# Performance work log

Measured on AMD Instinct MI355X. Metric: run time of the kernel, lower is better.

Reference implementation:

```python
import jax, jax.numpy as jnp
import numpy as np

B = 128      # number of swarms
NA = 64      # agents per swarm (na)
D = 8        # input feature dim
RD = 128     # attention hidden dim r
H = 16       # output channels h (l = sqrt(h) = 4)


def setup_inputs() -> dict:
    key = jax.random.key(0)
    ks = jax.random.split(key, 16)
    x = jax.random.normal(ks[0], (B * NA, D, NA), dtype=jnp.float32)
    L = jax.random.randint(ks[1], (B * NA, D, NA), 0, 2).astype(jnp.float32)
    p = lambda k, shp: jax.random.normal(k, shp, dtype=jnp.float32)
    return {
        "x": x, "L": L,
        "Aq": p(ks[2], (RD, D)), "Ak": p(ks[3], (RD, D)), "Av": p(ks[4], (RD, D)),
        "Aq1": p(ks[5], (RD, RD)), "Ak1": p(ks[6], (RD, RD)), "Av1": p(ks[7], (RD, RD)),
        "Aq5": p(ks[8], (RD, RD)), "Ak5": p(ks[9], (RD, RD)), "Av5": p(ks[10], (RD, RD)),
        "Ao": p(ks[11], (RD, RD)), "Ao1": p(ks[12], (RD, RD)), "Ao5": p(ks[13], (H, RD)),
    }


def _attn(Xin, Aq, Ak, Av, sqrt_nn):
    # Xin: (b, f, n); Aq/Ak/Av: (r, f); sqrt_nn: (b, 1, 1)
    Q = jax.nn.sigmoid(jnp.einsum('rf,bfn->bnr', Aq, Xin))   # Q already transposed
    K = jax.nn.sigmoid(jnp.einsum('rf,bfn->brn', Ak, Xin))
    V = jax.nn.sigmoid(jnp.einsum('rf,bfn->bnr', Av, Xin))
    S = jnp.einsum('bnr,brm->bnm', Q, K) / sqrt_nn           # (b, n, n)
    A = jax.nn.softmax(S, axis=2)
    return jnp.einsum('bnm,bmr->brn', A, V)                  # o^T: (b, r, n)


def _kron_eye2(A):
    # torch.kron(A, eye(2)) per batch: (B, n, n) -> (B, 2n, 2n)
    Bq, n, _ = A.shape
    I2 = jnp.eye(2, dtype=A.dtype)
    return (A[:, :, None, :, None] * I2[None, :, None, :]).reshape(Bq, 2 * n, 2 * n)


def reference(x, L, Aq, Ak, Av, Aq1, Ak1, Av1, Aq5, Ak5, Av5, Ao, Ao1, Ao5):
    na = x.shape[2]
    Bsw = x.shape[0] // na
    num_nb = jnp.sum((L[:, 0, :] >= 1.0).astype(jnp.float32), axis=1) + 1.0
    sqrt_nn = jnp.sqrt(num_nb)[:, None, None]                # (Bx, 1, 1)

    o = _attn(x, Aq, Ak, Av, sqrt_nn)
    R = jax.nn.silu(jnp.einsum('sr,brn->bsn', Ao, o))
    o = _attn(R, Aq1, Ak1, Av1, sqrt_nn)
    R = jax.nn.silu(jnp.einsum('sr,brn->bsn', Ao1, o))
    o = _attn(R, Aq5, Ak5, Av5, sqrt_nn)
    R = jax.nn.silu(jnp.einsum('hr,brn->bhn', Ao5, o))       # (Bx, 16, na)

    blk = lambda a, b: R[:, a:b, :].sum(axis=1).reshape(Bsw, na, na)
    R11 = _kron_eye2(blk(0, 4))
    R12 = _kron_eye2(blk(4, 8))
    R21 = _kron_eye2(blk(8, 12))
    R22 = _kron_eye2(blk(12, 16))
    # block matrix [[R11, R12], [R21, R22]] -> (Bsw, 4na, 4na)
    Rfull = jnp.concatenate(
        (jnp.concatenate((R11, R21), axis=1), jnp.concatenate((R12, R22), axis=1)),
        axis=2)

    Rfull = Rfull ** 2
    Rupper = Rfull + jnp.swapaxes(Rfull, 1, 2)
    n_tot = 4 * na
    Dg = jnp.eye(n_tot, dtype=Rupper.dtype)
    Rdiag = Rupper * (1.0 - Dg)                              # diag zeroed
    Rout = Dg * Rupper                                       # keep diag only
    rowsum = jnp.sum(Rdiag, axis=2)[:, :, None]              # (Bsw, n, 1)
    return Rout + Dg * rowsum - Rdiag
```

## Files before the change

kernel.cpp:

```cpp
#include <hip/hip_runtime.h>

typedef _Float16 f16;
typedef __attribute__((ext_vector_type(8))) _Float16 h8v;
typedef __attribute__((ext_vector_type(4))) float f4v;
typedef __attribute__((ext_vector_type(16))) float f16acc;

#define OFF_WQ  0
#define OFF_WK  2048
#define OFF_WV  4096
#define OFF_AQ1 6144
#define OFF_AK1 22528
#define OFF_AV1 38912
#define OFF_AQ5 55296
#define OFF_AK5 71680
#define OFF_AV5 88064
#define OFF_AO  104448
#define OFF_AO1 120832
#define OFF_AO5 137216
#define WTS_TOTAL 139264

#define P2 136
#define P1 72

__device__ __forceinline__ f4v mfma16_(h8v a, h8v b, f4v c) {
  return __builtin_amdgcn_mfma_f32_16x16x32_f16(a, b, c, 0, 0, 0);
}
__device__ __forceinline__ f16acc mfma32_(h8v a, h8v b, f16acc c) {
  return __builtin_amdgcn_mfma_f32_32x32x16_f16(a, b, c, 0, 0, 0);
}
__device__ __forceinline__ float rcp_(float x) { return __builtin_amdgcn_rcpf(x); }
__device__ __forceinline__ float ex2_(float x) {
#if __has_builtin(__builtin_amdgcn_exp2f)
  return __builtin_amdgcn_exp2f(x);
#else
  return __expf(x * 0.6931471805599453f);
#endif
}
__device__ __forceinline__ unsigned int pk2(float a, float b) {
  __fp16 __attribute__((ext_vector_type(2))) h2 = __builtin_amdgcn_cvt_pkrtz(a, b);
  return *reinterpret_cast<unsigned int*>(&h2);
}
__device__ __forceinline__ f16acc zero16() {
  f16acc z;
  #pragma unroll
  for (int i = 0; i < 16; ++i) z[i] = 0.f;
  return z;
}

template<int ACT>
__device__ __forceinline__ unsigned long long pack4act(float a, float b, float c, float d) {
  float v[4] = {a, b, c, d};
  #pragma unroll
  for (int j = 0; j < 4; ++j) {
    float t = v[j];
    if (ACT == 0)      t = rcp_(1.0f + ex2_(t));
    else if (ACT == 1) t = t * rcp_(1.0f + ex2_(t * -1.44269504f));
    v[j] = t;
  }
  union { unsigned long long u64; unsigned int u32[2]; } u;
  u.u32[0] = pk2(v[0], v[1]);
  u.u32[1] = pk2(v[2], v[3]);
  return u.u64;
}

template<int NKK>
__device__ __forceinline__ void qkv_ph(const f16* __restrict__ Wq,
                                       const f16* __restrict__ Wk,
                                       const f16* __restrict__ Wv,
                                       const f16* __restrict__ Xt,
                                       f16* __restrict__ Qt, f16* __restrict__ Kt,
                                       f16* __restrict__ Vb, int w, int lane)
{
  const int l31 = lane & 31, lh = lane >> 5;
  const int rt = w >> 1, ct = w & 1;
  const int xbase = (ct * 32 + l31) * P2 + lh * 8;
  f16acc aq = zero16(), ak = zero16(), av = zero16();
  #pragma unroll
  for (int kk = 0; kk < NKK; ++kk) {
    h8v xf = *(const h8v*)(Xt + xbase + kk * 16);
    const int fo = (rt * NKK + kk) * 512 + lane * 8;
    h8v fq = *(const h8v*)(Wq + fo);
    h8v fk = *(const h8v*)(Wk + fo);
    h8v fv = *(const h8v*)(Wv + fo);
    aq = mfma32_(fq, xf, aq);
    ak = mfma32_(fk, xf, ak);
    av = mfma32_(xf, fv, av);
  }
  const int nrow = (ct * 32 + l31) * P2;
  const int vrow = (rt * 32 + l31) * P1 + ct * 32 + lh * 4;
  #pragma unroll
  for (int q = 0; q < 4; ++q) {
    const int rr = rt * 32 + q * 8 + lh * 4;
    *(unsigned long long*)(Qt + nrow + rr) =
        pack4act<0>(aq[4*q], aq[4*q+1], aq[4*q+2], aq[4*q+3]);
    *(unsigned long long*)(Kt + nrow + rr) =
        pack4act<0>(ak[4*q], ak[4*q+1], ak[4*q+2], ak[4*q+3]);
    *(unsigned long long*)(Vb + vrow + q * 8) =
        pack4act<0>(av[4*q], av[4*q+1], av[4*q+2], av[4*q+3]);
  }
}

__device__ __forceinline__ void softmax_ph(const f16* __restrict__ Qt,
                                           const f16* __restrict__ Kt,
                                           f16* Ps, float* __restrict__ ssum,
                                           float is2, int w, int lane)
{
  const int lrow = lane & 15, lk = lane >> 4;
  const int nst = w & 3, mh = w >> 2;
  const int n = nst * 16 + lrow;
  h8v bq[4];
  #pragma unroll
  for (int kk = 0; kk < 4; ++kk)
    bq[kk] = *(const h8v*)(Qt + n * P2 + kk * 32 + lk * 8);
  f4v acc[2];
  #pragma unroll
  for (int t = 0; t < 2; ++t) {
    const int mt = mh * 2 + t;
    acc[t] = (f4v){0.f, 0.f, 0.f, 0.f};
    #pragma unroll
    for (int kk = 0; kk < 4; ++kk) {
      h8v a = *(const h8v*)(Kt + (mt * 16 + lrow) * P2 + kk * 32 + lk * 8);
      acc[t] = mfma16_(a, bq[kk], acc[t]);
    }
  }
  float sm = 0.f;
  #pragma unroll
  for (int t = 0; t < 2; ++t)
    #pragma unroll
    for (int j = 0; j < 4; ++j) { acc[t][j] = ex2_(acc[t][j] * is2); sm += acc[t][j]; }
  sm += __shfl_xor(sm, 16);
  sm += __shfl_xor(sm, 32);
  if (lk == 0) ssum[mh * 64 + n] = sm;
  __syncthreads();
  const float inv = rcp_(ssum[n] + ssum[64 + n]);
  #pragma unroll
  for (int t = 0; t < 2; ++t) {
    const int mt = mh * 2 + t;
    union { unsigned long long u64; unsigned int u32[2]; } u;
    u.u32[0] = pk2(acc[t][0] * inv, acc[t][1] * inv);
    u.u32[1] = pk2(acc[t][2] * inv, acc[t][3] * inv);
    *(unsigned long long*)(Ps + n * P1 + mt * 16 + lk * 4) = u.u64;
  }
}

__device__ __forceinline__ void pv_ph(const f16* __restrict__ Vb,
                                      const f16* __restrict__ Ps,
                                      f16* __restrict__ Ot, int w, int lane)
{
  const int l31 = lane & 31, lh = lane >> 5;
  const int rt = w >> 1, ct = w & 1;
  f16acc acc = zero16();
  #pragma unroll
  for (int kk = 0; kk < 4; ++kk) {
    h8v a = *(const h8v*)(Vb + (rt * 32 + l31) * P1 + kk * 16 + lh * 8);
    h8v b = *(const h8v*)(Ps + (ct * 32 + l31) * P1 + kk * 16 + lh * 8);
    acc = mfma32_(a, b, acc);
  }
  const int nrow = (ct * 32 + l31) * P2;
  #pragma unroll
  for (int q = 0; q < 4; ++q)
    *(unsigned long long*)(Ot + nrow + rt * 32 + q * 8 + lh * 4) =
        pack4act<2>(acc[4*q], acc[4*q+1], acc[4*q+2], acc[4*q+3]);
}

__device__ __forceinline__ void ao_ph(const f16* __restrict__ Ao,
                                      const f16* __restrict__ Ot,
                                      f16* __restrict__ Rt, int w, int lane)
{
  const int l31 = lane & 31, lh = lane >> 5;
  const int st = w >> 1, ct = w & 1;
  f16acc acc = zero16();
  #pragma unroll
  for (int kk = 0; kk < 8; ++kk) {
    h8v a = *(const h8v*)(Ao + (st * 8 + kk) * 512 + lane * 8);
    h8v b = *(const h8v*)(Ot + (ct * 32 + l31) * P2 + kk * 16 + lh * 8);
    acc = mfma32_(a, b, acc);
  }
  const int nrow = (ct * 32 + l31) * P2;
  #pragma unroll
  for (int q = 0; q < 4; ++q)
    *(unsigned long long*)(Rt + nrow + st * 32 + q * 8 + lh * 4) =
        pack4act<1>(acc[4*q], acc[4*q+1], acc[4*q+2], acc[4*q+3]);
}

__device__ __forceinline__ void final_ph(const f16* __restrict__ Ao5g,
                                         const f16* __restrict__ Ot,
                                         float* __restrict__ Mw, int b, int w, int lane)
{
  const int lrow = lane & 15, lk = lane >> 4;
  h8v a[4];
  #pragma unroll
  for (int kk = 0; kk < 4; ++kk)
    a[kk] = *(const h8v*)(Ao5g + lrow * 128 + kk * 32 + lk * 8);
  const int n = 16 * w + lrow;
  f4v acc = {0.f, 0.f, 0.f, 0.f};
  #pragma unroll
  for (int kk = 0; kk < 4; ++kk) {
    h8v bb = *(const h8v*)(Ot + n * P2 + kk * 32 + lk * 8);
    acc = mfma16_(a[kk], bb, acc);
  }
  float msum = 0.f;
  #pragma unroll
  for (int j = 0; j < 4; ++j) {
    float v = acc[j];
    v = v * rcp_(1.0f + ex2_(v * -1.44269504f));
    msum += v;
  }
  Mw[(size_t)(b >> 6) * 16384 + lk * 4096 + (b & 63) * 64 + n] = msum;
}

__global__ __launch_bounds__(512, 4)
void swarm_attn_mfma(const float* __restrict__ x, const float* __restrict__ L,
                     const f16* __restrict__ wts, float* __restrict__ Mw)
{
  __shared__ f16 Xt[64 * P2];
  __shared__ f16 Qt[64 * P2];
  __shared__ f16 Kt[64 * P2];
  __shared__ f16 Vb[128 * P1];
  __shared__ float ssum[2 * 64];
  f16* Ps = Xt;

  const int b = blockIdx.x;
  const int tid = threadIdx.x;
  const int w = tid >> 6, lane = tid & 63;

  {
    const int n = tid >> 3, c = tid & 7;
    unsigned int val = 0;
    if (c < 4) {
      const float a  = x[(size_t)b * 512 + (2 * c) * 64 + n];
      const float bb = x[(size_t)b * 512 + (2 * c + 1) * 64 + n];
      val = pk2(a, bb);
    }
    *(unsigned int*)(Xt + n * P2 + 2 * c) = val;
  }
  const float lv = L[(size_t)b * 512 + lane];
  const unsigned long long msk = __ballot(lv >= 1.0f);
  const float is2 = __frsqrt_rn((float)(__popcll(msk) + 1)) * 1.44269504f;
  __syncthreads();

  qkv_ph<1>(wts + OFF_WQ, wts + OFF_WK, wts + OFF_WV, Xt, Qt, Kt, Vb, w, lane);
  __syncthreads();
  softmax_ph(Qt, Kt, Ps, ssum, is2, w, lane);
  __syncthreads();
  pv_ph(Vb, Ps, Qt, w, lane);
  __syncthreads();
  ao_ph(wts + OFF_AO, Qt, Xt, w, lane);
  __syncthreads();

  qkv_ph<8>(wts + OFF_AQ1, wts + OFF_AK1, wts + OFF_AV1, Xt, Qt, Kt, Vb, w, lane);
  __syncthreads();
  softmax_ph(Qt, Kt, Ps, ssum, is2, w, lane);
  __syncthreads();
  pv_ph(Vb, Ps, Qt, w, lane);
  __syncthreads();
  ao_ph(wts + OFF_AO1, Qt, Xt, w, lane);
  __syncthreads();

  qkv_ph<8>(wts + OFF_AQ5, wts + OFF_AK5, wts + OFF_AV5, Xt, Qt, Kt, Vb, w, lane);
  __syncthreads();
  softmax_ph(Qt, Kt, Ps, ssum, is2, w, lane);
  __syncthreads();
  pv_ph(Vb, Ps, Qt, w, lane);
  __syncthreads();
  if (w < 4) final_ph(wts + OFF_AO5, Qt, Mw, b, w, lane);
}

__global__ void conv_wts(const float* Aq, const float* Ak, const float* Av,
                         const float* Aq1, const float* Ak1, const float* Av1,
                         const float* Aq5, const float* Ak5, const float* Av5,
                         const float* Ao, const float* Ao1, const float* Ao5,
                         f16* wts)
{
  const float SCL = -1.44269504088896f;
  const int t = blockIdx.x * 256 + threadIdx.x;
  if (t >= WTS_TOTAL) return;
  float v;
  if (t < 6144) {
    const int m = t >> 11, idx = t & 2047;
    const int fi = idx >> 9, rem = idx & 511, lane = rem >> 3, j = rem & 7;
    const int r = fi * 32 + (lane & 31), k = (lane >> 5) * 8 + j;
    const float* W = (m == 0) ? Aq : (m == 1) ? Ak : Av;
    v = (k < 8) ? W[r * 8 + k] * SCL : 0.f;
  } else if (t < 137216) {
    const int m = (t - 6144) >> 14, idx = (t - 6144) & 16383;
    const int fi = idx >> 9, rem = idx & 511, lane = rem >> 3, j = rem & 7;
    const int rt = fi >> 3, kk = fi & 7;
    const int r = rt * 32 + (lane & 31), k = kk * 16 + (lane >> 5) * 8 + j;
    const float* W = (m == 0) ? Aq1 : (m == 1) ? Ak1 : (m == 2) ? Av1 :
                     (m == 3) ? Aq5 : (m == 4) ? Ak5 : (m == 5) ? Av5 :
                     (m == 6) ? Ao : Ao1;
    v = W[r * 128 + k];
    if (m < 6) v *= SCL;
  } else {
    v = Ao5[t - 137216];
  }
  wts[t] = (f16)v;
}

__global__ __launch_bounds__(256, 4)
void reduce_kernel(const float* __restrict__ Mw, float* __restrict__ MwT,
                   float* __restrict__ rsw, float* __restrict__ csw)
{
  const int sg = blockIdx.x;
  const float* M = Mw + (size_t)sg * 4096;
  const int wv = threadIdx.x >> 6, l = threadIdx.x & 63;
  const int i = wv * 16 + (l & 15), q = l >> 4;
  float r2 = 0.f, c2 = 0.f;
  float colv[16];
  #pragma unroll
  for (int jj = 0; jj < 16; ++jj) {
    const float a = M[i * 64 + q * 16 + jj];
    r2 = fmaf(a, a, r2);
    const float bc = M[(q * 16 + jj) * 64 + i];
    c2 = fmaf(bc, bc, c2);
    colv[jj] = bc;
  }
  if (MwT) {
    float* MT = MwT + (size_t)sg * 4096 + i * 64 + q * 16;
    #pragma unroll
    for (int jj = 0; jj < 16; ++jj) MT[jj] = colv[jj];
  }
  r2 += __shfl_xor(r2, 16); r2 += __shfl_xor(r2, 32);
  c2 += __shfl_xor(c2, 16); c2 += __shfl_xor(c2, 32);
  if (q == 0) {
    const int s = sg >> 2, g = sg & 3;
    rsw[s * 256 + g * 64 + i] = r2;
    csw[s * 256 + g * 64 + i] = c2;
  }
}

__global__ __launch_bounds__(256, 1)
void expand_kernel(const float* __restrict__ Mw, const float* __restrict__ MwT,
                   const float* __restrict__ rsw, const float* __restrict__ csw,
                   float* __restrict__ out)
{
  const size_t e = ((size_t)blockIdx.x * 256 + threadIdx.x) * 4;
  const int s = (int)(e >> 16);
  const int rem = (int)(e & 65535);
  const int u = rem >> 8, v0 = rem & 255;
  const int ub = u >> 7, ii = (u & 127) >> 1, p = u & 1;
  const float* Ms = Mw + (size_t)s * 16384;
  const float* MsT = MwT ? MwT + (size_t)s * 16384 : nullptr;
  float4 o;
  float* po = &o.x;
  #pragma unroll
  for (int c = 0; c < 4; ++c) {
    const int v = v0 + c;
    const int vb = v >> 7, jj = (v & 127) >> 1, q = v & 1;
    float val = 0.f;
    if (u == v) {
      val = rsw[s * 256 + (2 * ub) * 64 + ii] + rsw[s * 256 + (2 * ub + 1) * 64 + ii]
          + csw[s * 256 + ub * 64 + ii] + csw[s * 256 + (2 + ub) * 64 + ii];
    } else if (p == q) {
      const int g = 2 * ub + vb, gp = 2 * vb + ub;
      const float a = Ms[g * 4096 + ii * 64 + jj];
      const float bb = MsT ? MsT[gp * 4096 + ii * 64 + jj]
                           : Ms[gp * 4096 + jj * 64 + ii];
      val = -(a * a + bb * bb);
    }
    po[c] = val;
  }
  *(float4*)(out + e) = o;
}

extern "C" void kernel_launch(void* const* d_in, const int* in_sizes, int n_in,
                              void* d_out, int out_size, void* d_ws, size_t ws_size,
                              hipStream_t stream)
{
  const float* x   = (const float*)d_in[0];
  const float* L   = (const float*)d_in[1];
  const float* Aq  = (const float*)d_in[2];
  const float* Ak  = (const float*)d_in[3];
  const float* Av  = (const float*)d_in[4];
  const float* Aq1 = (const float*)d_in[5];
  const float* Ak1 = (const float*)d_in[6];
  const float* Av1 = (const float*)d_in[7];
  const float* Aq5 = (const float*)d_in[8];
  const float* Ak5 = (const float*)d_in[9];
  const float* Av5 = (const float*)d_in[10];
  const float* Ao  = (const float*)d_in[11];
  const float* Ao1 = (const float*)d_in[12];
  const float* Ao5 = (const float*)d_in[13];

  f16* wts = (f16*)d_ws;
  float* Mw  = (float*)((char*)d_ws + (size_t)WTS_TOTAL * 2);
  float* rsw = Mw + (size_t)128 * 16384;
  float* csw = rsw + 128 * 256;
  float* MwT = csw + 128 * 256;
  const size_t need = (size_t)WTS_TOTAL * 2 +
                      ((size_t)128 * 16384 * 2 + 2 * 128 * 256) * sizeof(float);
  float* MwTp = (ws_size >= need) ? MwT : nullptr;

  conv_wts<<<(WTS_TOTAL + 255) / 256, 256, 0, stream>>>(Aq, Ak, Av, Aq1, Ak1, Av1,
                                                        Aq5, Ak5, Av5, Ao, Ao1, Ao5, wts);
  swarm_attn_mfma<<<8192, 512, 0, stream>>>(x, L, wts, Mw);
  reduce_kernel<<<512, 256, 0, stream>>>(Mw, MwTp, rsw, csw);
  expand_kernel<<<8192, 256, 0, stream>>>(Mw, MwTp, rsw, csw, (float*)d_out);
}
```

Measured before the change: 305.3 us.

## Process two swarm elements per block to share barriers and weight loads

Each 512-thread block now handles two batch elements, with every phase run back to back on both. The softmax is split into two halves so the second element's work sits between each pair of barriers, and the final projection divides the waves between the two elements. The aim is to amortise the many __syncthreads and global weight loads over twice the work and give the scheduler more independent instructions. The cost is doubled LDS per block, which limits occupancy (launch bounds changed to 1 block per CU), and higher register pressure from the interleaving.

Result: slower. 360.2 us (+18.0%).

```diff
diff --git a/kernel.cpp b/kernel.cpp
--- a/kernel.cpp
+++ b/kernel.cpp
@@ -100,10 +100,10 @@
   }
 }
 
-__device__ __forceinline__ void softmax_ph(const f16* __restrict__ Qt,
-                                           const f16* __restrict__ Kt,
-                                           f16* Ps, float* __restrict__ ssum,
-                                           float is2, int w, int lane)
+__device__ __forceinline__ void smA(const f16* __restrict__ Qt,
+                                    const f16* __restrict__ Kt,
+                                    float* __restrict__ ssum, f4v acc[2],
+                                    float is2, int w, int lane)
 {
   const int lrow = lane & 15, lk = lane >> 4;
   const int nst = w & 3, mh = w >> 2;
@@ -112,7 +112,6 @@
   #pragma unroll
   for (int kk = 0; kk < 4; ++kk)
     bq[kk] = *(const h8v*)(Qt + n * P2 + kk * 32 + lk * 8);
-  f4v acc[2];
   #pragma unroll
   for (int t = 0; t < 2; ++t) {
     const int mt = mh * 2 + t;
@@ -131,7 +130,14 @@
   sm += __shfl_xor(sm, 16);
   sm += __shfl_xor(sm, 32);
   if (lk == 0) ssum[mh * 64 + n] = sm;
-  __syncthreads();
+}
+
+__device__ __forceinline__ void smB(const float* __restrict__ ssum, f4v acc[2],
+                                    f16* __restrict__ Ps, int w, int lane)
+{
+  const int lrow = lane & 15, lk = lane >> 4;
+  const int nst = w & 3, mh = w >> 2;
+  const int n = nst * 16 + lrow;
   const float inv = rcp_(ssum[n] + ssum[64 + n]);
   #pragma unroll
   for (int t = 0; t < 2; ++t) {
@@ -185,14 +191,14 @@
 
 __device__ __forceinline__ void final_ph(const f16* __restrict__ Ao5g,
                                          const f16* __restrict__ Ot,
-                                         float* __restrict__ Mw, int b, int w, int lane)
+                                         float* __restrict__ Mw, int be, int ws, int lane)
 {
   const int lrow = lane & 15, lk = lane >> 4;
   h8v a[4];
   #pragma unroll
   for (int kk = 0; kk < 4; ++kk)
     a[kk] = *(const h8v*)(Ao5g + lrow * 128 + kk * 32 + lk * 8);
-  const int n = 16 * w + lrow;
+  const int n = 16 * ws + lrow;
   f4v acc = {0.f, 0.f, 0.f, 0.f};
   #pragma unroll
   for (int kk = 0; kk < 4; ++kk) {
@@ -206,64 +212,88 @@
     v = v * rcp_(1.0f + ex2_(v * -1.44269504f));
     msum += v;
   }
-  Mw[(size_t)(b >> 6) * 16384 + lk * 4096 + (b & 63) * 64 + n] = msum;
-}
-
-__global__ __launch_bounds__(512, 4)
+  Mw[(size_t)(be >> 6) * 16384 + lk * 4096 + (be & 63) * 64 + n] = msum;
+}
+
+__global__ __launch_bounds__(512, 1)
 void swarm_attn_mfma(const float* __restrict__ x, const float* __restrict__ L,
                      const f16* __restrict__ wts, float* __restrict__ Mw)
 {
-  __shared__ f16 Xt[64 * P2];
-  __shared__ f16 Qt[64 * P2];
-  __shared__ f16 Kt[64 * P2];
-  __shared__ f16 Vb[128 * P1];
-  __shared__ float ssum[2 * 64];
-  f16* Ps = Xt;
-
-  const int b = blockIdx.x;
+  __shared__ f16 Xt[2][64 * P2];
+  __shared__ f16 Qt[2][64 * P2];
+  __shared__ f16 Kt[2][64 * P2];
+  __shared__ f16 Vb[2][128 * P1];
+  __shared__ float ssum[2][128];
+
+  const int b0 = blockIdx.x * 2;
   const int tid = threadIdx.x;
   const int w = tid >> 6, lane = tid & 63;
 
-  {
+  #pragma unroll
+  for (int e = 0; e < 2; ++e) {
     const int n = tid >> 3, c = tid & 7;
     unsigned int val = 0;
     if (c < 4) {
-      const float a  = x[(size_t)b * 512 + (2 * c) * 64 + n];
-      const float bb = x[(size_t)b * 512 + (2 * c + 1) * 64 + n];
+      const float a  = x[(size_t)(b0 + e) * 512 + (2 * c) * 64 + n];
+      const float bb = x[(size_t)(b0 + e) * 512 + (2 * c + 1) * 64 + n];
       val = pk2(a, bb);
     }
-    *(unsigned int*)(Xt + n * P2 + 2 * c) = val;
-  }
-  const float lv = L[(size_t)b * 512 + lane];
-  const unsigned long long msk = __ballot(lv >= 1.0f);
-  const float is2 = __frsqrt_rn((float)(__popcll(msk) + 1)) * 1.44269504f;
-  __syncthreads();
-
-  qkv_ph<1>(wts + OFF_WQ, wts + OFF_WK, wts + OFF_WV, Xt, Qt, Kt, Vb, w, lane);
-  __syncthreads();
-  softmax_ph(Qt, Kt, Ps, ssum, is2, w, lane);
-  __syncthreads();
-  pv_ph(Vb, Ps, Qt, w, lane);
-  __syncthreads();
-  ao_ph(wts + OFF_AO, Qt, Xt, w, lane);
-  __syncthreads();
-
-  qkv_ph<8>(wts + OFF_AQ1, wts + OFF_AK1, wts + OFF_AV1, Xt, Qt, Kt, Vb, w, lane);
-  __syncthreads();
-  softmax_ph(Qt, Kt, Ps, ssum, is2, w, lane);
-  __syncthreads();
-  pv_ph(Vb, Ps, Qt, w, lane);
-  __syncthreads();
-  ao_ph(wts + OFF_AO1, Qt, Xt, w, lane);
-  __syncthreads();
-
-  qkv_ph<8>(wts + OFF_AQ5, wts + OFF_AK5, wts + OFF_AV5, Xt, Qt, Kt, Vb, w, lane);
-  __syncthreads();
-  softmax_ph(Qt, Kt, Ps, ssum, is2, w, lane);
-  __syncthreads();
-  pv_ph(Vb, Ps, Qt, w, lane);
-  __syncthreads();
-  if (w < 4) final_ph(wts + OFF_AO5, Qt, Mw, b, w, lane);
+    *(unsigned int*)(&Xt[e][0] + n * P2 + 2 * c) = val;
+  }
+  const float lv0 = L[(size_t)b0 * 512 + lane];
+  const float is2_0 = __frsqrt_rn((float)(__popcll(__ballot(lv0 >= 1.0f)) + 1)) * 1.44269504f;
+  const float lv1 = L[(size_t)(b0 + 1) * 512 + lane];
+  const float is2_1 = __frsqrt_rn((float)(__popcll(__ballot(lv1 >= 1.0f)) + 1)) * 1.44269504f;
+  __syncthreads();
+
+  f4v a0[2], a1[2];
+
+  qkv_ph<1>(wts + OFF_WQ, wts + OFF_WK, wts + OFF_WV, Xt[0], Qt[0], Kt[0], Vb[0], w, lane);
+  qkv_ph<1>(wts + OFF_WQ, wts + OFF_WK, wts + OFF_WV, Xt[1], Qt[1], Kt[1], Vb[1], w, lane);
+  __syncthreads();
+  smA(Qt[0], Kt[0], ssum[0], a0, is2_0, w, lane);
+  smA(Qt[1], Kt[1], ssum[1], a1, is2_1, w, lane);
+  __syncthreads();
+  smB(ssum[0], a0, Xt[0], w, lane);
+  smB(ssum[1], a1, Xt[1], w, lane);
+  __syncthreads();
+  pv_ph(Vb[0], Xt[0], Qt[0], w, lane);
+  pv_ph(Vb[1], Xt[1], Qt[1], w, lane);
+  __syncthreads();
+  ao_ph(wts + OFF_AO, Qt[0], Xt[0], w, lane);
+  ao_ph(wts + OFF_AO, Qt[1], Xt[1], w, lane);
+  __syncthreads();
+
+  qkv_ph<8>(wts + OFF_AQ1, wts + OFF_AK1, wts + OFF_AV1, Xt[0], Qt[0], Kt[0], Vb[0], w, lane);
+  qkv_ph<8>(wts + OFF_AQ1, wts + OFF_AK1, wts + OFF_AV1, Xt[1], Qt[1], Kt[1], Vb[1], w, lane);
+  __syncthreads();
+  smA(Qt[0], Kt[0], ssum[0], a0, is2_0, w, lane);
+  smA(Qt[1], Kt[1], ssum[1], a1, is2_1, w, lane);
+  __syncthreads();
+  smB(ssum[0], a0, Xt[0], w, lane);
+  smB(ssum[1], a1, Xt[1], w, lane);
+  __syncthreads();
+  pv_ph(Vb[0], Xt[0], Qt[0], w, lane);
+  pv_ph(Vb[1], Xt[1], Qt[1], w, lane);
+  __syncthreads();
+  ao_ph(wts + OFF_AO1, Qt[0], Xt[0], w, lane);
+  ao_ph(wts + OFF_AO1, Qt[1], Xt[1], w, lane);
+  __syncthreads();
+
+  qkv_ph<8>(wts + OFF_AQ5, wts + OFF_AK5, wts + OFF_AV5, Xt[0], Qt[0], Kt[0], Vb[0], w, lane);
+  qkv_ph<8>(wts + OFF_AQ5, wts + OFF_AK5, wts + OFF_AV5, Xt[1], Qt[1], Kt[1], Vb[1], w, lane);
+  __syncthreads();
+  smA(Qt[0], Kt[0], ssum[0], a0, is2_0, w, lane);
+  smA(Qt[1], Kt[1], ssum[1], a1, is2_1, w, lane);
+  __syncthreads();
+  smB(ssum[0], a0, Xt[0], w, lane);
+  smB(ssum[1], a1, Xt[1], w, lane);
+  __syncthreads();
+  pv_ph(Vb[0], Xt[0], Qt[0], w, lane);
+  pv_ph(Vb[1], Xt[1], Qt[1], w, lane);
+  __syncthreads();
+  if (w < 4) final_ph(wts + OFF_AO5, Qt[0], Mw, b0, w, lane);
+  else       final_ph(wts + OFF_AO5, Qt[1], Mw, b0 + 1, w - 4, lane);
 }
 
 __global__ void conv_wts(const float* Aq, const float* Ak, const float* Av,
@@ -394,7 +424,7 @@
 
   conv_wts<<<(WTS_TOTAL + 255) / 256, 256, 0, stream>>>(Aq, Ak, Av, Aq1, Ak1, Av1,
                                                         Aq5, Ak5, Av5, Ao, Ao1, Ao5, wts);
-  swarm_attn_mfma<<<8192, 512, 0, stream>>>(x, L, wts, Mw);
+  swarm_attn_mfma<<<4096, 512, 0, stream>>>(x, L, wts, Mw);
   reduce_kernel<<<512, 256, 0, stream>>>(Mw, MwTp, rsw, csw);
   expand_kernel<<<8192, 256, 0, stream>>>(Mw, MwTp, rsw, csw, (float*)d_out);
 }
```
